# Kernel optimization log

Measured on AMD Instinct MI355X. Metric: run time of the kernel, lower is better.

## Reference

```python
import jax, jax.numpy as jnp
import numpy as np

B, C, H, W = 4, 3, 512, 960
K2 = 16  # 4x4 adaptive filter, DAIN-style


def setup_inputs() -> dict:
    key = jax.random.key(0)
    k1, k2, k3 = jax.random.split(key, 3)
    teninput = jax.random.normal(k1, (B, C, H, W), dtype=jnp.float32)
    tenflow = jax.random.normal(k2, (B, 2, H, W), dtype=jnp.float32)
    tenfilter = jax.random.uniform(k3, (B, K2, H, W), dtype=jnp.float32)
    return {"teninput": teninput, "tenflow": tenflow, "tenfilter": tenfilter}


def reference(teninput, tenflow, tenfilter):
    # DAIN FilterInterpolation forward:
    # out[b,c,y,x] = valid * sum_{dj,di < K} filter[b, dj*K+di, y, x]
    #               * bilinear(input, y2_T + dj + beta, x2_L + di + alpha)
    # with per-corner clamped gathers; out-of-bounds flow targets give 0.
    b, c, h, w = teninput.shape
    k2 = tenfilter.shape[1]
    K = int(np.sqrt(k2))

    dt = teninput.dtype
    xs = jnp.arange(w, dtype=dt)[None, None, :]
    ys = jnp.arange(h, dtype=dt)[None, :, None]
    fx, fy = tenflow[:, 0], tenflow[:, 1]          # [B,H,W]
    x2 = xs + fx
    y2 = ys + fy
    valid = ((x2 >= 0) & (x2 <= w - 1) & (y2 >= 0) & (y2 <= h - 1)
             & (jnp.abs(fx) < w / 2) & (jnp.abs(fy) < h / 2))

    ix = jnp.floor(x2).astype(jnp.int32)
    iy = jnp.floor(y2).astype(jnp.int32)
    alpha = (x2 - ix)[:, None]                     # [B,1,H,W]
    beta = (y2 - iy)[:, None]
    ixL0 = ix + 1 - K // 2                         # window left edge
    iyT0 = iy + 1 - K // 2                         # window top edge

    inp_flat = teninput.reshape(b, c, h * w)

    def gather(yi, xi):  # yi, xi: [B,H,W] int -> [B,C,H,W]
        idx = (yi * w + xi).reshape(b, 1, h * w)
        return jnp.take_along_axis(inp_flat, idx, axis=2).reshape(b, c, h, w)

    wTL = (1 - alpha) * (1 - beta)
    wTR = alpha * (1 - beta)
    wBL = (1 - alpha) * beta
    wBR = alpha * beta

    out = jnp.zeros_like(teninput)
    for dj in range(K):
        yT = jnp.clip(iyT0 + dj, 0, h - 1)
        yB = jnp.clip(iyT0 + dj + 1, 0, h - 1)
        for di in range(K):
            xL = jnp.clip(ixL0 + di, 0, w - 1)
            xR = jnp.clip(ixL0 + di + 1, 0, w - 1)
            val = (wTL * gather(yT, xL) + wTR * gather(yT, xR)
                   + wBL * gather(yB, xL) + wBR * gather(yB, xR))
            out = out + val * tenfilter[:, dj * K + di][:, None]

    return out * valid[:, None].astype(dt)
```

## Files before the change

kernel.cpp:

```cpp
#include <hip/hip_runtime.h>

#define BB 4
#define CC 3
#define HH 512
#define WW 960
#define HW (HH * WW)
#define NPIX (BB * HW)

__global__ __launch_bounds__(256)
void filter_interp_kernel(const float* __restrict__ inp,
                          const float* __restrict__ flow,
                          const float* __restrict__ filt,
                          float* __restrict__ out) {
    int tid = blockIdx.x * blockDim.x + threadIdx.x;
    if (tid >= NPIX) return;

    int b   = tid / HW;
    int rem = tid - b * HW;
    int y   = rem / WW;
    int x   = rem - y * WW;

    const float fx = flow[(b * 2 + 0) * HW + rem];
    const float fy = flow[(b * 2 + 1) * HW + rem];
    const float x2 = (float)x + fx;
    const float y2 = (float)y + fy;

    bool valid = (x2 >= 0.0f) && (x2 <= (float)(WW - 1)) &&
                 (y2 >= 0.0f) && (y2 <= (float)(HH - 1)) &&
                 (fabsf(fx) < (float)WW * 0.5f) &&
                 (fabsf(fy) < (float)HH * 0.5f);

    const int outbase = b * CC * HW + rem;
    if (!valid) {
        out[outbase]          = 0.0f;
        out[outbase + HW]     = 0.0f;
        out[outbase + 2 * HW] = 0.0f;
        return;
    }

    const int ix = (int)floorf(x2);
    const int iy = (int)floorf(y2);
    const float alpha = x2 - (float)ix;
    const float beta  = y2 - (float)iy;

    const float wTL = (1.0f - alpha) * (1.0f - beta);
    const float wTR = alpha * (1.0f - beta);
    const float wBL = (1.0f - alpha) * beta;
    const float wBR = alpha * beta;

    const int ixL0 = ix - 1;
    const int iyT0 = iy - 1;

    int R[5];
#pragma unroll
    for (int j = 0; j < 5; ++j) R[j] = min(max(iyT0 + j, 0), HH - 1);

    float Wm[5][5];
#pragma unroll
    for (int j = 0; j < 5; ++j)
#pragma unroll
        for (int i = 0; i < 5; ++i) Wm[j][i] = 0.0f;

    const float* fptr = filt + (size_t)b * 16 * HW + rem;
#pragma unroll
    for (int dj = 0; dj < 4; ++dj) {
#pragma unroll
        for (int di = 0; di < 4; ++di) {
            const float f = fptr[(size_t)(dj * 4 + di) * HW];
            Wm[dj][di]         += f * wTL;
            Wm[dj][di + 1]     += f * wTR;
            Wm[dj + 1][di]     += f * wBL;
            Wm[dj + 1][di + 1] += f * wBR;
        }
    }

    const float* ibase = inp + (size_t)b * CC * HW;
    float acc[3] = {0.0f, 0.0f, 0.0f};

    if (ixL0 >= 0 && ixL0 + 4 <= WW - 1) {
        const int a0 = ixL0 & ~3;
        const int o  = ixL0 - a0;

        const bool s2 = (o & 2) != 0;
        const bool s1 = (o & 1) != 0;
        float We[5][8];
#pragma unroll
        for (int j = 0; j < 5; ++j) {
            float t[8];
#pragma unroll
            for (int i = 0; i < 8; ++i) t[i] = (i < 5) ? Wm[j][i] : 0.0f;
            float u[8];
#pragma unroll
            for (int i = 0; i < 8; ++i)
                u[i] = s2 ? ((i >= 2) ? t[i - 2] : 0.0f) : t[i];
#pragma unroll
            for (int i = 0; i < 8; ++i)
                We[j][i] = s1 ? ((i >= 1) ? u[i - 1] : 0.0f) : u[i];
        }

#pragma unroll
        for (int j = 0; j < 5; ++j) {
            const size_t rowoff = (size_t)R[j] * WW + a0;
#pragma unroll
            for (int c = 0; c < CC; ++c) {
                const float* rp = ibase + (size_t)c * HW + rowoff;
                const float4 p0 = *(const float4*)(rp);
                const float4 p1 = *(const float4*)(rp + 4);
                float a = acc[c];
                a += p0.x * We[j][0];
                a += p0.y * We[j][1];
                a += p0.z * We[j][2];
                a += p0.w * We[j][3];
                a += p1.x * We[j][4];
                a += p1.y * We[j][5];
                a += p1.z * We[j][6];
                a += p1.w * We[j][7];
                acc[c] = a;
            }
        }
    } else {
        int S[5];
#pragma unroll
        for (int i = 0; i < 5; ++i) S[i] = min(max(ixL0 + i, 0), WW - 1);
#pragma unroll
        for (int c = 0; c < CC; ++c) {
            const float* ic = ibase + (size_t)c * HW;
            float a = 0.0f;
#pragma unroll
            for (int j = 0; j < 5; ++j) {
                const float* row = ic + (size_t)R[j] * WW;
#pragma unroll
                for (int i = 0; i < 5; ++i) a += row[S[i]] * Wm[j][i];
            }
            acc[c] = a;
        }
    }

    out[outbase]          = acc[0];
    out[outbase + HW]     = acc[1];
    out[outbase + 2 * HW] = acc[2];
}

extern "C" void kernel_launch(void* const* d_in, const int* in_sizes, int n_in,
                              void* d_out, int out_size, void* d_ws, size_t ws_size,
                              hipStream_t stream) {
    const float* teninput  = (const float*)d_in[0];
    const float* tenflow   = (const float*)d_in[1];
    const float* tenfilter = (const float*)d_in[2];
    float* out = (float*)d_out;

    const int threads = 256;
    const int blocks  = (NPIX + threads - 1) / threads;
    filter_interp_kernel<<<blocks, threads, 0, stream>>>(teninput, tenflow, tenfilter, out);
}
```

Baseline: 241.1 us.

## Stage input halo tiles in LDS for per-block 2D tiles with swizzled block order

Each block now handles a 64x4 pixel tile and first loads a 16-row by 80-column halo of all three input channels into shared memory. Pixels whose 5x5 window falls inside that halo read from LDS, and the rest fall back to clamped global gathers. Block indices are swizzled across eight groups, and the 16 filter taps are preloaded before the barrier so their latency overlaps with the LDS fill. The flow is random normal, so most windows land within a few pixels and should hit LDS. The cost is staging a halo far larger than the tile (16 rows for 4 output rows) plus a block-wide sync.

```diff
diff --git a/kernel.cpp b/kernel.cpp
--- a/kernel.cpp
+++ b/kernel.cpp
@@ -7,138 +7,167 @@
 #define HW (HH * WW)
 #define NPIX (BB * HW)
 
+#define TW 64
+#define TH 4
+#define NTX (WW / TW)
+#define NTY (HH / TH)
+#define NBLK (BB * NTX * NTY)
+
+#define ROWS 16
+#define COLS 80
+#define CPAD 84
+#define LDS_FLOATS (ROWS * CC * CPAD)
+
 __global__ __launch_bounds__(256)
 void filter_interp_kernel(const float* __restrict__ inp,
                           const float* __restrict__ flow,
                           const float* __restrict__ filt,
                           float* __restrict__ out) {
-    int tid = blockIdx.x * blockDim.x + threadIdx.x;
-    if (tid >= NPIX) return;
+    __shared__ float lds[LDS_FLOATS];
 
-    int b   = tid / HW;
-    int rem = tid - b * HW;
-    int y   = rem / WW;
-    int x   = rem - y * WW;
+    const int bid = blockIdx.x;
+    const int swz = (bid & 7) * (NBLK / 8) + (bid >> 3);
+    const int b   = swz / (NTX * NTY);
+    const int rr  = swz - b * (NTX * NTY);
+    const int tx  = rr / NTY;
+    const int ty  = rr - tx * NTY;
+    const int x0  = tx * TW;
+    const int y0  = ty * TH;
 
-    const float fx = flow[(b * 2 + 0) * HW + rem];
-    const float fy = flow[(b * 2 + 1) * HW + rem];
+    const int tid = threadIdx.x;
+    const float* ibase = inp + (size_t)b * CC * HW;
+
+    if (tx > 0 && tx < NTX - 1) {
+#pragma unroll
+        for (int e = 0; e < 4; ++e) {
+            const int idx = e * 256 + tid;
+            if (idx < ROWS * CC * (COLS / 4)) {
+                const int s  = idx / (CC * (COLS / 4));
+                const int r2 = idx - s * (CC * (COLS / 4));
+                const int ch = r2 / (COLS / 4);
+                const int t4 = r2 - ch * (COLS / 4);
+                const int grow = min(max(y0 - 5 + s, 0), HH - 1);
+                const float4 v = *(const float4*)(ibase + (size_t)ch * HW +
+                                                  (size_t)grow * WW +
+                                                  (x0 - 8 + t4 * 4));
+                *(float4*)&lds[(s * CC + ch) * CPAD + t4 * 4] = v;
+            }
+        }
+    } else {
+#pragma unroll
+        for (int e = 0; e < 15; ++e) {
+            const int idx = e * 256 + tid;
+            const int s  = idx / (CC * COLS);
+            const int r2 = idx - s * (CC * COLS);
+            const int ch = r2 / COLS;
+            const int t  = r2 - ch * COLS;
+            const int grow = min(max(y0 - 5 + s, 0), HH - 1);
+            const int gcol = min(max(x0 - 8 + t, 0), WW - 1);
+            lds[(s * CC + ch) * CPAD + t] =
+                ibase[(size_t)ch * HW + (size_t)grow * WW + gcol];
+        }
+    }
+
+    const int lx = tid & (TW - 1);
+    const int wy = tid >> 6;
+    const int x  = x0 + lx;
+    const int y  = y0 + wy;
+    const int rem = y * WW + x;
+
+    const float fx = flow[(size_t)(b * 2 + 0) * HW + rem];
+    const float fy = flow[(size_t)(b * 2 + 1) * HW + rem];
+
+    float f[16];
+    {
+        const float* fptr = filt + (size_t)b * 16 * HW + rem;
+#pragma unroll
+        for (int k = 0; k < 16; ++k) f[k] = fptr[(size_t)k * HW];
+    }
+
+    __syncthreads();
+
     const float x2 = (float)x + fx;
     const float y2 = (float)y + fy;
 
-    bool valid = (x2 >= 0.0f) && (x2 <= (float)(WW - 1)) &&
-                 (y2 >= 0.0f) && (y2 <= (float)(HH - 1)) &&
-                 (fabsf(fx) < (float)WW * 0.5f) &&
-                 (fabsf(fy) < (float)HH * 0.5f);
+    const bool valid = (x2 >= 0.0f) && (x2 <= (float)(WW - 1)) &&
+                       (y2 >= 0.0f) && (y2 <= (float)(HH - 1)) &&
+                       (fabsf(fx) < (float)WW * 0.5f) &&
+                       (fabsf(fy) < (float)HH * 0.5f);
 
-    const int outbase = b * CC * HW + rem;
-    if (!valid) {
-        out[outbase]          = 0.0f;
-        out[outbase + HW]     = 0.0f;
-        out[outbase + 2 * HW] = 0.0f;
-        return;
-    }
+    float acc0 = 0.0f, acc1 = 0.0f, acc2 = 0.0f;
 
-    const int ix = (int)floorf(x2);
-    const int iy = (int)floorf(y2);
-    const float alpha = x2 - (float)ix;
-    const float beta  = y2 - (float)iy;
+    if (valid) {
+        const int ix = (int)floorf(x2);
+        const int iy = (int)floorf(y2);
+        const float alpha = x2 - (float)ix;
+        const float beta  = y2 - (float)iy;
 
-    const float wTL = (1.0f - alpha) * (1.0f - beta);
-    const float wTR = alpha * (1.0f - beta);
-    const float wBL = (1.0f - alpha) * beta;
-    const float wBR = alpha * beta;
+        const float wTL = (1.0f - alpha) * (1.0f - beta);
+        const float wTR = alpha * (1.0f - beta);
+        const float wBL = (1.0f - alpha) * beta;
+        const float wBR = alpha * beta;
 
-    const int ixL0 = ix - 1;
-    const int iyT0 = iy - 1;
+        float Wm[5][5];
+#pragma unroll
+        for (int j = 0; j < 5; ++j)
+#pragma unroll
+            for (int i = 0; i < 5; ++i) Wm[j][i] = 0.0f;
+#pragma unroll
+        for (int dj = 0; dj < 4; ++dj) {
+#pragma unroll
+            for (int di = 0; di < 4; ++di) {
+                const float fv = f[dj * 4 + di];
+                Wm[dj][di]         += fv * wTL;
+                Wm[dj][di + 1]     += fv * wTR;
+                Wm[dj + 1][di]     += fv * wBL;
+                Wm[dj + 1][di + 1] += fv * wBR;
+            }
+        }
 
-    int R[5];
+        const int ixL0 = ix - 1;
+        const int iyT0 = iy - 1;
+        const int cs = ixL0 - (x0 - 8);
+        const int rs = iyT0 - (y0 - 5);
+
+        if ((unsigned)rs <= (unsigned)(ROWS - 5) &&
+            (unsigned)cs <= (unsigned)(COLS - 5)) {
+            const float* lbase = &lds[rs * (CC * CPAD) + cs];
 #pragma unroll
-    for (int j = 0; j < 5; ++j) R[j] = min(max(iyT0 + j, 0), HH - 1);
-
-    float Wm[5][5];
+            for (int j = 0; j < 5; ++j) {
+                const float* lr = lbase + j * (CC * CPAD);
 #pragma unroll
-    for (int j = 0; j < 5; ++j)
+                for (int i = 0; i < 5; ++i) {
+                    const float w = Wm[j][i];
+                    acc0 += lr[i] * w;
+                    acc1 += lr[CPAD + i] * w;
+                    acc2 += lr[2 * CPAD + i] * w;
+                }
+            }
+        } else {
+            int R[5], S[5];
 #pragma unroll
-        for (int i = 0; i < 5; ++i) Wm[j][i] = 0.0f;
-
-    const float* fptr = filt + (size_t)b * 16 * HW + rem;
+            for (int j = 0; j < 5; ++j) R[j] = min(max(iyT0 + j, 0), HH - 1);
 #pragma unroll
-    for (int dj = 0; dj < 4; ++dj) {
+            for (int i = 0; i < 5; ++i) S[i] = min(max(ixL0 + i, 0), WW - 1);
 #pragma unroll
-        for (int di = 0; di < 4; ++di) {
-            const float f = fptr[(size_t)(dj * 4 + di) * HW];
-            Wm[dj][di]         += f * wTL;
-            Wm[dj][di + 1]     += f * wTR;
-            Wm[dj + 1][di]     += f * wBL;
-            Wm[dj + 1][di + 1] += f * wBR;
+            for (int j = 0; j < 5; ++j) {
+                const float* r0 = ibase + (size_t)R[j] * WW;
+#pragma unroll
+                for (int i = 0; i < 5; ++i) {
+                    const float w = Wm[j][i];
+                    const size_t o = (size_t)S[i];
+                    acc0 += r0[o] * w;
+                    acc1 += r0[HW + o] * w;
+                    acc2 += r0[2 * (size_t)HW + o] * w;
+                }
+            }
         }
     }
 
-    const float* ibase = inp + (size_t)b * CC * HW;
-    float acc[3] = {0.0f, 0.0f, 0.0f};
-
-    if (ixL0 >= 0 && ixL0 + 4 <= WW - 1) {
-        const int a0 = ixL0 & ~3;
-        const int o  = ixL0 - a0;
-
-        const bool s2 = (o & 2) != 0;
-        const bool s1 = (o & 1) != 0;
-        float We[5][8];
-#pragma unroll
-        for (int j = 0; j < 5; ++j) {
-            float t[8];
-#pragma unroll
-            for (int i = 0; i < 8; ++i) t[i] = (i < 5) ? Wm[j][i] : 0.0f;
-            float u[8];
-#pragma unroll
-            for (int i = 0; i < 8; ++i)
-                u[i] = s2 ? ((i >= 2) ? t[i - 2] : 0.0f) : t[i];
-#pragma unroll
-            for (int i = 0; i < 8; ++i)
-                We[j][i] = s1 ? ((i >= 1) ? u[i - 1] : 0.0f) : u[i];
-        }
-
-#pragma unroll
-        for (int j = 0; j < 5; ++j) {
-            const size_t rowoff = (size_t)R[j] * WW + a0;
-#pragma unroll
-            for (int c = 0; c < CC; ++c) {
-                const float* rp = ibase + (size_t)c * HW + rowoff;
-                const float4 p0 = *(const float4*)(rp);
-                const float4 p1 = *(const float4*)(rp + 4);
-                float a = acc[c];
-                a += p0.x * We[j][0];
-                a += p0.y * We[j][1];
-                a += p0.z * We[j][2];
-                a += p0.w * We[j][3];
-                a += p1.x * We[j][4];
-                a += p1.y * We[j][5];
-                a += p1.z * We[j][6];
-                a += p1.w * We[j][7];
-                acc[c] = a;
-            }
-        }
-    } else {
-        int S[5];
-#pragma unroll
-        for (int i = 0; i < 5; ++i) S[i] = min(max(ixL0 + i, 0), WW - 1);
-#pragma unroll
-        for (int c = 0; c < CC; ++c) {
-            const float* ic = ibase + (size_t)c * HW;
-            float a = 0.0f;
-#pragma unroll
-            for (int j = 0; j < 5; ++j) {
-                const float* row = ic + (size_t)R[j] * WW;
-#pragma unroll
-                for (int i = 0; i < 5; ++i) a += row[S[i]] * Wm[j][i];
-            }
-            acc[c] = a;
-        }
-    }
-
-    out[outbase]          = acc[0];
-    out[outbase + HW]     = acc[1];
-    out[outbase + 2 * HW] = acc[2];
+    const int outbase = b * CC * HW + rem;
+    out[outbase]          = acc0;
+    out[outbase + HW]     = acc1;
+    out[outbase + 2 * HW] = acc2;
 }
 
 extern "C" void kernel_launch(void* const* d_in, const int* in_sizes, int n_in,
@@ -149,7 +178,5 @@
     const float* tenfilter = (const float*)d_in[2];
     float* out = (float*)d_out;
 
-    const int threads = 256;
-    const int blocks  = (NPIX + threads - 1) / threads;
-    filter_interp_kernel<<<blocks, threads, 0, stream>>>(teninput, tenflow, tenfilter, out);
+    filter_interp_kernel<<<NBLK, 256, 0, stream>>>(teninput, tenflow, tenfilter, out);
 }
```

New measurement: 227.2 us. 5.8% less time.
